# Performance work log

Measured on AMD Instinct MI355X. Metric: run time of the kernel, lower is better.

The kernel has to match this reference:

```python
import jax, jax.numpy as jnp
import numpy as np

B, S, D_IN, D_OUT, H = 4096, 128, 64, 128, 32


def setup_inputs() -> dict:
    key = jax.random.key(0)
    ks = jax.random.split(key, 8)
    x = jax.random.normal(ks[0], (B, S, D_IN), dtype=jnp.float32)
    mask = jax.random.bernoulli(ks[1], 0.7, (B, S))  # bool [B,S]
    # token-wise encoder ('net') params
    W_net = jax.random.normal(ks[2], (D_IN, D_OUT), dtype=jnp.float32) / np.sqrt(D_IN)
    b_net = jnp.zeros((D_OUT,), dtype=jnp.float32)
    # jet_to_top MLP: Linear(D_OUT,32) -> ReLU -> Linear(32,4)
    W1 = jax.random.normal(ks[3], (D_OUT, H), dtype=jnp.float32) / np.sqrt(D_OUT)
    b1 = jnp.zeros((H,), dtype=jnp.float32)
    W2 = jax.random.normal(ks[4], (H, 4), dtype=jnp.float32) / np.sqrt(H)
    b2 = jnp.zeros((4,), dtype=jnp.float32)
    return {"x": x, "W_net": W_net, "b_net": b_net,
            "W1": W1, "b1": b1, "W2": W2, "b2": b2, "mask": mask}


def reference(x, W_net, b_net, W1, b1, W2, b2, mask):
    # net: token-wise encoder -> [B, S, D_OUT]
    t_out = jnp.einsum('bsd,dh->bsh', x, W_net) + b_net

    # indices of first two valid jets per sample (stable sort pushes False last)
    idx = jnp.argsort(~mask, axis=1, stable=True)[:, :2]           # [B, 2]
    n_valid = mask.sum(axis=1)                                     # [B]

    feats = jnp.take_along_axis(t_out, idx[:, :, None], axis=1)    # [B, 2, D_OUT]

    # jet_to_top MLP on the two gathered jets
    h = jax.nn.relu(jnp.einsum('bkd,dh->bkh', feats, W1) + b1)
    preds = jnp.einsum('bkh,ho->bko', h, W2) + b2                  # [B, 2, 4]

    nv = n_valid[:, None]                                          # [B, 1]
    zero = jnp.zeros_like(preds[:, 0])
    top1 = jnp.where(nv >= 1, preds[:, 0], zero)
    top2 = jnp.where(nv >= 2, preds[:, 1], jnp.where(nv == 1, preds[:, 0], zero))
    return jnp.stack([top1, top2], axis=1)                         # [B, 2, 4]
```

## Files before the change

kernel.cpp:

```cpp
#include <hip/hip_runtime.h>

#define BATCH 4096
#define SEQ   128
#define DIN   64
#define DOUT  128
#define HID   32

__global__ __launch_bounds__(64) void fused_mlp_topk_kernel(
    const float* __restrict__ x,
    const float* __restrict__ Wn,
    const float* __restrict__ bn,
    const float* __restrict__ W1,
    const float* __restrict__ b1,
    const float* __restrict__ W2,
    const float* __restrict__ b2,
    const int*   __restrict__ mask,
    float*       __restrict__ out)
{
    const int b    = blockIdx.x;
    const int lane = threadIdx.x;

    const int m0 = mask[b * SEQ + lane];
    const int m1 = mask[b * SEQ + 64 + lane];
    const unsigned long long bal0 = __ballot(m0 != 0);
    const unsigned long long bal1 = __ballot(m1 != 0);

    int i0 = 0, i1 = 0, cnt = 0;
    if (bal0) {
        i0 = __builtin_ctzll(bal0);
        unsigned long long rem = bal0 & (bal0 - 1ull);
        if (rem)       { i1 = __builtin_ctzll(rem);       cnt = 2; }
        else if (bal1) { i1 = 64 + __builtin_ctzll(bal1); cnt = 2; }
        else           { i1 = i0;                         cnt = 1; }
    } else if (bal1) {
        i0 = 64 + __builtin_ctzll(bal1);
        unsigned long long rem = bal1 & (bal1 - 1ull);
        if (rem) { i1 = 64 + __builtin_ctzll(rem); cnt = 2; }
        else     { i1 = i0;                        cnt = 1; }
    }

    const size_t xbase = (size_t)b * SEQ * DIN;
    const float x0 = x[xbase + (size_t)i0 * DIN + lane];
    const float x1 = x[xbase + (size_t)i1 * DIN + lane];

    float f00 = bn[lane], f01 = bn[lane + 64];
    float f10 = f00,      f11 = f01;
    #pragma unroll 8
    for (int d = 0; d < DIN; ++d) {
        const float w0 = Wn[d * DOUT + lane];
        const float w1 = Wn[d * DOUT + 64 + lane];
        const float xa = __shfl(x0, d);
        const float xb = __shfl(x1, d);
        f00 = fmaf(xa, w0, f00);
        f01 = fmaf(xa, w1, f01);
        f10 = fmaf(xb, w0, f10);
        f11 = fmaf(xb, w1, f11);
    }

    __shared__ float feats[2][DOUT];
    feats[0][lane]      = f00;
    feats[0][lane + 64] = f01;
    feats[1][lane]      = f10;
    feats[1][lane + 64] = f11;
    __syncthreads();

    const int r = lane >> 5;
    const int k = lane & 31;
    float h = b1[k];
    #pragma unroll 8
    for (int j = 0; j < DOUT; ++j) {
        h = fmaf(feats[r][j], W1[j * HID + k], h);
    }
    h = fmaxf(h, 0.0f);

    __shared__ float hsm[2][HID];
    hsm[r][k] = h;
    __syncthreads();

    if (lane < 8) {
        const int rr = lane >> 2;
        const int o  = lane & 3;
        float p = b2[o];
        #pragma unroll
        for (int kk = 0; kk < HID; ++kk) {
            p = fmaf(hsm[rr][kk], W2[kk * 4 + o], p);
        }
        out[b * 8 + lane] = (cnt >= 1) ? p : 0.0f;
    }
}

extern "C" void kernel_launch(void* const* d_in, const int* in_sizes, int n_in,
                              void* d_out, int out_size, void* d_ws, size_t ws_size,
                              hipStream_t stream) {
    const float* x    = (const float*)d_in[0];
    const float* Wn   = (const float*)d_in[1];
    const float* bn   = (const float*)d_in[2];
    const float* W1   = (const float*)d_in[3];
    const float* b1   = (const float*)d_in[4];
    const float* W2   = (const float*)d_in[5];
    const float* b2   = (const float*)d_in[6];
    const int*   mask = (const int*)d_in[7];
    float* out = (float*)d_out;

    fused_mlp_topk_kernel<<<BATCH, 64, 0, stream>>>(x, Wn, bn, W1, b1, W2, b2, mask, out);
}
```

Baseline: 183.4 us.

## Fold encoder and first MLP layer weights into a single precomputed matrix

Adds a prep kernel that multiplies the token encoder weights by the first MLP layer weights, folding both biases into the workspace. The main kernel then applies one 64x32 projection per selected jet instead of a 64x128 layer followed by a 128x32 layer. The second MLP layer becomes a wave-level shuffle reduction with no shared memory or barriers. It adds an extra kernel launch and changes float rounding order slightly.

```diff
diff --git a/kernel.cpp b/kernel.cpp
--- a/kernel.cpp
+++ b/kernel.cpp
@@ -6,15 +6,39 @@
 #define DOUT  128
 #define HID   32
 
-__global__ __launch_bounds__(64) void fused_mlp_topk_kernel(
-    const float* __restrict__ x,
+
+__global__ __launch_bounds__(256) void prep_fold_kernel(
     const float* __restrict__ Wn,
     const float* __restrict__ bn,
     const float* __restrict__ W1,
     const float* __restrict__ b1,
+    float*       __restrict__ ws)
+{
+    const int t = blockIdx.x * 256 + threadIdx.x;
+    if (t < DIN * HID) {
+        const int d = t >> 5;
+        const int k = t & (HID - 1);
+        float s = 0.0f;
+        #pragma unroll 8
+        for (int j = 0; j < DOUT; ++j)
+            s = fmaf(Wn[d * DOUT + j], W1[j * HID + k], s);
+        ws[t] = s;
+    } else if (t < DIN * HID + HID) {
+        const int k = t - DIN * HID;
+        float s = b1[k];
+        #pragma unroll 8
+        for (int j = 0; j < DOUT; ++j)
+            s = fmaf(bn[j], W1[j * HID + k], s);
+        ws[t] = s;
+    }
+}
+
+__global__ __launch_bounds__(64) void fused_mlp_topk_kernel(
+    const float* __restrict__ x,
+    const int*   __restrict__ mask,
     const float* __restrict__ W2,
     const float* __restrict__ b2,
-    const int*   __restrict__ mask,
+    const float* __restrict__ ws,
     float*       __restrict__ out)
 {
     const int b    = blockIdx.x;
@@ -39,53 +63,40 @@
         else     { i1 = i0;                        cnt = 1; }
     }
 
-    const size_t xbase = (size_t)b * SEQ * DIN;
-    const float x0 = x[xbase + (size_t)i0 * DIN + lane];
-    const float x1 = x[xbase + (size_t)i1 * DIN + lane];
-
-    float f00 = bn[lane], f01 = bn[lane + 64];
-    float f10 = f00,      f11 = f01;
-    #pragma unroll 8
-    for (int d = 0; d < DIN; ++d) {
-        const float w0 = Wn[d * DOUT + lane];
-        const float w1 = Wn[d * DOUT + 64 + lane];
-        const float xa = __shfl(x0, d);
-        const float xb = __shfl(x1, d);
-        f00 = fmaf(xa, w0, f00);
-        f01 = fmaf(xa, w1, f01);
-        f10 = fmaf(xb, w0, f10);
-        f11 = fmaf(xb, w1, f11);
-    }
-
-    __shared__ float feats[2][DOUT];
-    feats[0][lane]      = f00;
-    feats[0][lane + 64] = f01;
-    feats[1][lane]      = f10;
-    feats[1][lane + 64] = f11;
-    __syncthreads();
-
     const int r = lane >> 5;
     const int k = lane & 31;
-    float h = b1[k];
+    const int isel = r ? i1 : i0;
+
+    const size_t xrow = (size_t)b * SEQ * DIN + (size_t)isel * DIN;
+    const float xlo = x[xrow + k];
+    const float xhi = x[xrow + 32 + k];
+
+    float h = ws[DIN * HID + k];
     #pragma unroll 8
-    for (int j = 0; j < DOUT; ++j) {
-        h = fmaf(feats[r][j], W1[j * HID + k], h);
+    for (int d = 0; d < 32; ++d) {
+        const float xa = __shfl(xlo, d, 32);
+        const float xb = __shfl(xhi, d, 32);
+        h = fmaf(xa, ws[d * HID + k], h);
+        h = fmaf(xb, ws[(d + 32) * HID + k], h);
     }
     h = fmaxf(h, 0.0f);
 
-    __shared__ float hsm[2][HID];
-    hsm[r][k] = h;
-    __syncthreads();
+    float p0 = h * W2[k * 4 + 0];
+    float p1 = h * W2[k * 4 + 1];
+    float p2 = h * W2[k * 4 + 2];
+    float p3 = h * W2[k * 4 + 3];
+    #pragma unroll
+    for (int off = 16; off > 0; off >>= 1) {
+        p0 += __shfl_xor(p0, off, 32);
+        p1 += __shfl_xor(p1, off, 32);
+        p2 += __shfl_xor(p2, off, 32);
+        p3 += __shfl_xor(p3, off, 32);
+    }
 
-    if (lane < 8) {
-        const int rr = lane >> 2;
-        const int o  = lane & 3;
-        float p = b2[o];
-        #pragma unroll
-        for (int kk = 0; kk < HID; ++kk) {
-            p = fmaf(hsm[rr][kk], W2[kk * 4 + o], p);
-        }
-        out[b * 8 + lane] = (cnt >= 1) ? p : 0.0f;
+    if (k < 4) {
+        float p = (k == 0) ? p0 : (k == 1) ? p1 : (k == 2) ? p2 : p3;
+        p += b2[k];
+        out[b * 8 + r * 4 + k] = (cnt >= 1) ? p : 0.0f;
     }
 }
 
@@ -101,6 +112,8 @@
     const float* b2   = (const float*)d_in[6];
     const int*   mask = (const int*)d_in[7];
     float* out = (float*)d_out;
+    float* ws  = (float*)d_ws;
 
-    fused_mlp_topk_kernel<<<BATCH, 64, 0, stream>>>(x, Wn, bn, W1, b1, W2, b2, mask, out);
+    prep_fold_kernel<<<(DIN * HID + HID + 255) / 256, 256, 0, stream>>>(Wn, bn, W1, b1, ws);
+    fused_mlp_topk_kernel<<<BATCH, 64, 0, stream>>>(x, mask, W2, b2, ws, out);
 }
```

Result: no change. 183.5 us (+0.1%).
